# Performance work log

Hardware: AMD Instinct MI355X
Metric: run time of the kernel (lower is better)

The kernel has to match this reference:

```python
import jax, jax.numpy as jnp
import numpy as np

GAMMA = 0.002  # Gaussian kernel bandwidth (init_kwargs)


def setup_inputs() -> dict:
    key = jax.random.key(0)
    k1, k2 = jax.random.split(key)
    x = jax.random.normal(k1, (4096, 512), dtype=jnp.float32)   # queries [B, D]
    sv = jax.random.normal(k2, (8192, 512), dtype=jnp.float32)  # centers [N, D]
    return {"x": x, "sv": sv}


def reference(x, sv):
    # Gaussian (RBF) kernel matrix: K[b, n] = exp(-gamma * ||x_b - sv_n||^2)
    # original chunked broadcast-subtract-square loop (same math, fused).
    x2 = jnp.sum(x * x, axis=-1)            # [B]
    s2 = jnp.sum(sv * sv, axis=-1)          # [N]
    cross = jnp.einsum('bd,nd->bn', x, sv)  # [B, N]
    d2 = x2[:, None] + s2[None, :] - 2.0 * cross
    return jnp.exp(-GAMMA * d2)
```

## Files before the change

kernel.cpp:

```cpp
#include <hip/hip_runtime.h>
#include <hip/hip_bf16.h>
#include <stdint.h>

#define GAMMA 0.002f
#define MDIM 4096
#define NDIM 8192
#define KDIM 512
#define BM 128
#define BN 128
#define BK 32

typedef short v8s  __attribute__((ext_vector_type(8)));
typedef float v16f __attribute__((ext_vector_type(16)));

__device__ __forceinline__ unsigned short f32_to_bf16_rne(float f) {
    union { float f; uint32_t u; } v; v.f = f;
    uint32_t u = v.u;
    return (unsigned short)((u + 0x7fffu + ((u >> 16) & 1u)) >> 16);
}

__device__ __forceinline__ void gl_lds16(const void* g, void* l) {
    __builtin_amdgcn_global_load_lds(
        (const __attribute__((address_space(1))) uint32_t*)g,
        (__attribute__((address_space(3))) uint32_t*)l, 16, 0, 0);
}

__global__ __launch_bounds__(256) void convert_all(
    const float* __restrict__ x, const float* __restrict__ sv,
    unsigned short* __restrict__ xb, unsigned short* __restrict__ svb,
    float* __restrict__ arow, float* __restrict__ ccol) {
    int row = blockIdx.x;
    const float* src;
    unsigned short* dst;
    float* red_out;
    if (row < MDIM) {
        src = x + (size_t)row * KDIM;
        dst = xb + (size_t)row * KDIM;
        red_out = arow + row;
    } else {
        int r = row - MDIM;
        src = sv + (size_t)r * KDIM;
        dst = svb + (size_t)r * KDIM;
        red_out = ccol + r;
    }
    int t = threadIdx.x;
    float2 f = ((const float2*)src)[t];
    ushort2 b;
    b.x = f32_to_bf16_rne(f.x);
    b.y = f32_to_bf16_rne(f.y);
    ((ushort2*)dst)[t] = b;
    float s = f.x * f.x + f.y * f.y;
    #pragma unroll
    for (int off = 32; off > 0; off >>= 1) s += __shfl_down(s, off, 64);
    __shared__ float red[4];
    if ((t & 63) == 0) red[t >> 6] = s;
    __syncthreads();
    if (t == 0) *red_out = -GAMMA * (red[0] + red[1] + red[2] + red[3]);
}

__global__ __launch_bounds__(256) void rbf_gemm(
    const unsigned short* __restrict__ A,
    const unsigned short* __restrict__ B,
    const float* __restrict__ arow,
    const float* __restrict__ ccol,
    float* __restrict__ out) {

    __shared__ __align__(16) unsigned short sA[BM * BK];
    __shared__ __align__(16) unsigned short sB[BN * BK];

    const int tid  = threadIdx.x;
    const int lane = tid & 63;
    const int wave = tid >> 6;
    const int wm   = wave >> 1;
    const int wn   = wave & 1;
    const int row0 = blockIdx.y * BM;
    const int col0 = blockIdx.x * BN;

    const int srow = tid >> 2;
    const int sch  = (tid & 3) ^ (srow & 3);
    const unsigned short* aptr = A + (size_t)(row0 + srow) * KDIM + sch * 8;
    const unsigned short* bptr = B + (size_t)(col0 + srow) * KDIM + sch * 8;
    unsigned short* sAp = &sA[tid * 8];
    unsigned short* sBp = &sB[tid * 8];

    v16f acc[2][2];
    #pragma unroll
    for (int i = 0; i < 2; i++)
        #pragma unroll
        for (int j = 0; j < 2; j++) acc[i][j] = (v16f)0.0f;

    const int r32 = lane & 31;
    const int kh  = lane >> 5;
    const int sw  = r32 & 3;

    for (int k0 = 0; k0 < KDIM; k0 += BK) {
        gl_lds16(aptr + k0, sAp);
        gl_lds16(aptr + (size_t)64 * KDIM + k0, sAp + 2048);
        gl_lds16(bptr + k0, sBp);
        gl_lds16(bptr + (size_t)64 * KDIM + k0, sBp + 2048);
        __syncthreads();

        v8s af[2][2], bf[2][2];
        #pragma unroll
        for (int ks = 0; ks < 2; ks++) {
            const int ch = ((ks * 2 + kh) ^ sw) * 8;
            #pragma unroll
            for (int i = 0; i < 2; i++) {
                af[i][ks] = *(const v8s*)&sA[(wm * 64 + i * 32 + r32) * BK + ch];
                bf[i][ks] = *(const v8s*)&sB[(wn * 64 + i * 32 + r32) * BK + ch];
            }
        }
        #pragma unroll
        for (int ks = 0; ks < 2; ks++)
            #pragma unroll
            for (int i = 0; i < 2; i++)
                #pragma unroll
                for (int j = 0; j < 2; j++)
                    acc[i][j] = __builtin_amdgcn_mfma_f32_32x32x16_bf16(
                        af[i][ks], bf[j][ks], acc[i][j], 0, 0, 0);
        __syncthreads();
    }

    float* fA = (float*)sA;
    float* fC = (float*)sB;
    if (tid < 128) fA[tid] = arow[row0 + tid];
    else           fC[tid - 128] = ccol[col0 + tid - 128];
    __syncthreads();

    const float tg = 2.0f * GAMMA;
    #pragma unroll
    for (int i = 0; i < 2; i++) {
        #pragma unroll
        for (int j = 0; j < 2; j++) {
            const int cl = wn * 64 + j * 32 + r32;
            const float cc = fC[cl];
            #pragma unroll
            for (int reg = 0; reg < 16; reg++) {
                const int rr = wm * 64 + i * 32 + (reg & 3) + 8 * (reg >> 2) + 4 * kh;
                out[(size_t)(row0 + rr) * NDIM + (col0 + cl)] =
                    __expf(fmaf(tg, acc[i][j][reg], fA[rr] + cc));
            }
        }
    }
}

extern "C" void kernel_launch(void* const* d_in, const int* in_sizes, int n_in,
                              void* d_out, int out_size, void* d_ws, size_t ws_size,
                              hipStream_t stream) {
    const float* x  = (const float*)d_in[0];
    const float* sv = (const float*)d_in[1];
    float* out = (float*)d_out;

    unsigned short* xb  = (unsigned short*)d_ws;
    unsigned short* svb = xb + (size_t)MDIM * KDIM;
    float* arow = (float*)(svb + (size_t)NDIM * KDIM);
    float* ccol = arow + MDIM;

    hipLaunchKernelGGL(convert_all, dim3(MDIM + NDIM), dim3(256), 0, stream,
                       x, sv, xb, svb, arow, ccol);
    hipLaunchKernelGGL(rbf_gemm, dim3(NDIM / BN, MDIM / BM), dim3(256), 0, stream,
                       xb, svb, arow, ccol, out);
}
```

Baseline: 194.4 us.

## Double-buffer LDS tiles in RBF GEMM and preload bias before main loop

The shared-memory A/B tiles become two ping-pong buffers, so the next K-slice is fetched with global_load_lds while the current slice feeds the MFMAs. This leaves one barrier per iteration instead of two. The row and column bias values move into their own shared array loaded before the main loop, which removes the extra barrier and reload in the epilogue. The cost is twice the LDS for tiles, which could lower occupancy, and how much the loads overlap depends on where the compiler places its wait before each barrier.

```diff
diff --git a/kernel.cpp b/kernel.cpp
--- a/kernel.cpp
+++ b/kernel.cpp
@@ -9,6 +9,7 @@
 #define BM 128
 #define BN 128
 #define BK 32
+#define KITERS (KDIM / BK)
 
 typedef short v8s  __attribute__((ext_vector_type(8)));
 typedef float v16f __attribute__((ext_vector_type(16)));
@@ -65,8 +66,9 @@
     const float* __restrict__ ccol,
     float* __restrict__ out) {
 
-    __shared__ __align__(16) unsigned short sA[BM * BK];
-    __shared__ __align__(16) unsigned short sB[BN * BK];
+    __shared__ __align__(16) unsigned short sA[2][BM * BK];
+    __shared__ __align__(16) unsigned short sB[2][BN * BK];
+    __shared__ float sBias[BM + BN];
 
     const int tid  = threadIdx.x;
     const int lane = tid & 63;
@@ -76,12 +78,13 @@
     const int row0 = blockIdx.y * BM;
     const int col0 = blockIdx.x * BN;
 
+    if (tid < BM) sBias[tid] = arow[row0 + tid];
+    else          sBias[tid] = ccol[col0 + tid - BM];
+
     const int srow = tid >> 2;
     const int sch  = (tid & 3) ^ (srow & 3);
     const unsigned short* aptr = A + (size_t)(row0 + srow) * KDIM + sch * 8;
     const unsigned short* bptr = B + (size_t)(col0 + srow) * KDIM + sch * 8;
-    unsigned short* sAp = &sA[tid * 8];
-    unsigned short* sBp = &sB[tid * 8];
 
     v16f acc[2][2];
     #pragma unroll
@@ -93,12 +96,24 @@
     const int kh  = lane >> 5;
     const int sw  = r32 & 3;
 
-    for (int k0 = 0; k0 < KDIM; k0 += BK) {
-        gl_lds16(aptr + k0, sAp);
-        gl_lds16(aptr + (size_t)64 * KDIM + k0, sAp + 2048);
-        gl_lds16(bptr + k0, sBp);
-        gl_lds16(bptr + (size_t)64 * KDIM + k0, sBp + 2048);
+    gl_lds16(aptr, &sA[0][tid * 8]);
+    gl_lds16(aptr + (size_t)64 * KDIM, &sA[0][tid * 8 + 2048]);
+    gl_lds16(bptr, &sB[0][tid * 8]);
+    gl_lds16(bptr + (size_t)64 * KDIM, &sB[0][tid * 8 + 2048]);
+
+    #pragma unroll
+    for (int k = 0; k < KITERS; ++k) {
+        const int cur = k & 1;
+        const int nxt = cur ^ 1;
         __syncthreads();
+
+        if (k + 1 < KITERS) {
+            const int k0 = (k + 1) * BK;
+            gl_lds16(aptr + k0, &sA[nxt][tid * 8]);
+            gl_lds16(aptr + (size_t)64 * KDIM + k0, &sA[nxt][tid * 8 + 2048]);
+            gl_lds16(bptr + k0, &sB[nxt][tid * 8]);
+            gl_lds16(bptr + (size_t)64 * KDIM + k0, &sB[nxt][tid * 8 + 2048]);
+        }
 
         v8s af[2][2], bf[2][2];
         #pragma unroll
@@ -106,8 +121,8 @@
             const int ch = ((ks * 2 + kh) ^ sw) * 8;
             #pragma unroll
             for (int i = 0; i < 2; i++) {
-                af[i][ks] = *(const v8s*)&sA[(wm * 64 + i * 32 + r32) * BK + ch];
-                bf[i][ks] = *(const v8s*)&sB[(wn * 64 + i * 32 + r32) * BK + ch];
+                af[i][ks] = *(const v8s*)&sA[cur][(wm * 64 + i * 32 + r32) * BK + ch];
+                bf[i][ks] = *(const v8s*)&sB[cur][(wn * 64 + i * 32 + r32) * BK + ch];
             }
         }
         #pragma unroll
@@ -118,15 +133,10 @@
                 for (int j = 0; j < 2; j++)
                     acc[i][j] = __builtin_amdgcn_mfma_f32_32x32x16_bf16(
                         af[i][ks], bf[j][ks], acc[i][j], 0, 0, 0);
-        __syncthreads();
     }
 
-    float* fA = (float*)sA;
-    float* fC = (float*)sB;
-    if (tid < 128) fA[tid] = arow[row0 + tid];
-    else           fC[tid - 128] = ccol[col0 + tid - 128];
-    __syncthreads();
-
+    const float* fA = sBias;
+    const float* fC = sBias + BM;
     const float tg = 2.0f * GAMMA;
     #pragma unroll
     for (int i = 0; i < 2; i++) {
```

Result: faster. 189.3 us (-2.6%).
